# Performance work log

Hardware: AMD Instinct MI355X
Metric: run time of the kernel (lower is better)

Reference implementation:

```python
import jax, jax.numpy as jnp
import numpy as np

WINDOW = (2, 8, 8)  # (T, H, W); N = 128
NUM_HEADS = 6
DIM = 192


def _relative_position_index(ws):
    """NxN int index into the relative-position-bias table (faithful port)."""
    d, h, w = np.meshgrid(np.arange(ws[0]), np.arange(ws[1]), np.arange(ws[2]), indexing='ij')
    coords = np.stack([d, h, w]).reshape(3, -1)            # (3, N)
    rel = coords[:, :, None] - coords[:, None, :]          # (3, N, N)
    rel = rel.transpose(1, 2, 0).astype(np.int64)          # (N, N, 3)
    rel[:, :, 0] += ws[0] - 1
    rel[:, :, 1] += ws[1] - 1
    rel[:, :, 2] += ws[2] - 1
    rel[:, :, 0] *= (2 * ws[1] - 1) * (2 * ws[2] - 1)
    rel[:, :, 1] *= 2 * ws[2] - 1
    return rel.sum(-1)                                     # (N, N)


def setup_inputs() -> dict:
    key = jax.random.key(0)
    k1, k2, k3, k4, k5, k6 = jax.random.split(key, 6)
    N = WINDOW[0] * WINDOW[1] * WINDOW[2]                  # 128
    B_ = 1024                                              # num_windows * batch
    nW = 64
    table_len = (2 * WINDOW[0] - 1) * (2 * WINDOW[1] - 1) * (2 * WINDOW[2] - 1)  # 675
    x = jax.random.normal(k1, (B_, N, DIM), dtype=jnp.float32)
    mask = jax.random.normal(k2, (nW, N, N), dtype=jnp.float32)  # additive attn mask
    qkv_w = jax.random.normal(k3, (3 * DIM, DIM), dtype=jnp.float32) * 0.02
    proj_w = jax.random.normal(k4, (DIM, DIM), dtype=jnp.float32) * 0.02
    proj_b = jax.random.normal(k5, (DIM,), dtype=jnp.float32) * 0.02
    rpb_table = jax.random.normal(k6, (table_len, NUM_HEADS), dtype=jnp.float32) * 0.02
    rel_index = jnp.asarray(_relative_position_index(WINDOW), dtype=jnp.int32)
    return {"x": x, "mask": mask, "qkv_w": qkv_w, "proj_w": proj_w,
            "proj_b": proj_b, "rpb_table": rpb_table, "rel_index": rel_index}


def reference(x, mask, qkv_w, proj_w, proj_b, rpb_table, rel_index):
    B_, N, C = x.shape
    H = NUM_HEADS
    hd = C // H
    scale = hd ** (-0.5)
    # qkv projection (no bias, qkv_bias=False)
    qkv = (x @ qkv_w.T).reshape(B_, N, 3, H, hd)
    q, k, v = qkv[:, :, 0], qkv[:, :, 1], qkv[:, :, 2]      # (B_, N, H, hd)
    # windowed attention scores
    attn = jnp.einsum('bnhd,bmhd->bhnm', q * scale, k)      # (B_, H, N, N)
    # gathered relative-position bias: (N, N, H) -> (H, N, N)
    bias = rpb_table[rel_index.reshape(-1)].reshape(N, N, H).transpose(2, 0, 1)
    attn = attn + bias[None]
    # shift-window mask: (nW, N, N) broadcast over batch groups and heads
    nW = mask.shape[0]
    attn = attn.reshape(B_ // nW, nW, H, N, N) + mask[None, :, None]
    attn = attn.reshape(B_, H, N, N)
    attn = jax.nn.softmax(attn, axis=-1)
    out = jnp.einsum('bhnm,bmhd->bnhd', attn, v).reshape(B_, N, C)
    return out @ proj_w.T + proj_b
```

## Files before the change

kernel.cpp:

```cpp
#include <hip/hip_runtime.h>
#include <hip/hip_bf16.h>


typedef float f32x4 __attribute__((ext_vector_type(4)));
typedef short short8 __attribute__((ext_vector_type(8)));
typedef short short4e __attribute__((ext_vector_type(4)));

#define SCALE 0.17677669529663687f
#define LOG2E 1.4426950408889634f
#define QSC (SCALE * LOG2E)

static __device__ __forceinline__ short f2bf(float f) {
  __hip_bfloat16 h = __float2bfloat16(f);
  return __builtin_bit_cast(short, h);
}
static __device__ __forceinline__ f32x4 mfma16(short8 a, short8 b, f32x4 c) {
  return __builtin_amdgcn_mfma_f32_16x16x32_bf16(a, b, c, 0, 0, 0);
}

__global__ __launch_bounds__(256) void prep_w(const float* __restrict__ qkvw,
                                              const float* __restrict__ projw,
                                              short* __restrict__ wbf,
                                              short* __restrict__ pwbf) {
  int t = blockIdx.x * 256 + threadIdx.x;
  const int NQ = 27648;
  float4 f; short* dst;
  if (t < NQ) { f = ((const float4*)qkvw)[t]; dst = wbf + t * 4; }
  else        { f = ((const float4*)projw)[t - NQ]; dst = pwbf + (t - NQ) * 4; }
  short4e o; o[0] = f2bf(f.x); o[1] = f2bf(f.y); o[2] = f2bf(f.z); o[3] = f2bf(f.w);
  *(short4e*)dst = o;
}

__global__ __launch_bounds__(256) void prep_bm(const int* __restrict__ rel,
                                               const float* __restrict__ table,
                                               const float* __restrict__ mask,
                                               float* __restrict__ bmF) {
  int blk = blockIdx.x;
  int h = blk >> 6, w = blk & 63;
  int tid = threadIdx.x, lane = tid & 63, wave = tid >> 6;
  int lr = lane & 15, r4 = (lane >> 4) * 4;
  const float* mk = mask + (size_t)w * 16384;
  float* dst = bmF + (size_t)blk * 16384;
#pragma unroll
  for (int L = 0; L < 16; ++L) {
    int rf = L >> 3, rg = (L >> 1) & 3, cp = L & 1;
    int row = wave * 32 + rf * 16 + r4 + rg;
    float4 v;
#pragma unroll
    for (int e = 0; e < 4; ++e) {
      int col = (cp * 4 + e) * 16 + lr;
      float bias = table[rel[row * 128 + col] * 6 + h];
      ((float*)&v)[e] = (bias + mk[row * 128 + col]) * LOG2E;
    }
    ((float4*)dst)[L * 256 + tid] = v;
  }
}

__global__ __launch_bounds__(256, 2) void qkv_kernel(const float* __restrict__ x,
                                                     const short* __restrict__ wbf,
                                                     short* __restrict__ qb,
                                                     short* __restrict__ kb,
                                                     short* __restrict__ vb) {
  __shared__ short xt[24576];
  __shared__ short wt[2][6144];
  const int b = blockIdx.x, tid = threadIdx.x;
  const int wave = tid >> 6, lane = tid & 63;
  const int lr = lane & 15, g = lane >> 4;
  const int g16 = g * 16, r4 = g * 4;
  const int rowbase = wave * 32;
  const int xorkey = (lr & 7) << 4;
  char* xtb = (char*)xt;
  char* wtb = (char*)wt;

  int wsoff[3], wdoff[3];
#pragma unroll
  for (int i = 0; i < 3; ++i) {
    int idx8 = i * 256 + tid;
    int r = idx8 / 24, c = idx8 - r * 24;
    wsoff[i] = idx8 * 8;
    wdoff[i] = r * 384 + ((c * 16) ^ ((r & 7) << 4));
  }
  short8 wreg[3];
#pragma unroll
  for (int i = 0; i < 3; ++i) wreg[i] = *(const short8*)(wbf + wsoff[i]);

  const float4* xr = (const float4*)(x + (size_t)b * 24576);
  for (int s = tid; s < 6144; s += 256) {
    float4 f = xr[s];
    int r = s / 48, c8 = s - r * 48;
    int off = r * 384 + ((c8 * 8) ^ ((r & 7) << 4));
    short4e o; o[0] = f2bf(f.x); o[1] = f2bf(f.y); o[2] = f2bf(f.z); o[3] = f2bf(f.w);
    *(short4e*)(xtb + off) = o;
  }
#pragma unroll
  for (int i = 0; i < 3; ++i) *(short8*)(wtb + wdoff[i]) = wreg[i];
  __syncthreads();

  const int rA0 = (rowbase + lr) * 384, rA1 = rA0 + 16 * 384;
  const int wB0 = lr * 384, wB1 = wB0 + 16 * 384;

  for (int ch = 0; ch < 18; ++ch) {
    if (ch < 17) {
#pragma unroll
      for (int i = 0; i < 3; ++i)
        wreg[i] = *(const short8*)(wbf + (ch + 1) * 6144 + wsoff[i]);
    }
    const char* wbuf = wtb + (ch & 1) * 12288;
    f32x4 acc[2][2];
    acc[0][0] = acc[0][1] = acc[1][0] = acc[1][1] = f32x4{0.f, 0.f, 0.f, 0.f};
    const bool isv = (ch >= 12);
#pragma unroll
    for (int ks = 0; ks < 6; ++ks) {
      int cx = (ks * 64 + g16) ^ xorkey;
      short8 xa0 = *(const short8*)(xtb + rA0 + cx);
      short8 xa1 = *(const short8*)(xtb + rA1 + cx);
      short8 wf0 = *(const short8*)(wbuf + wB0 + cx);
      short8 wf1 = *(const short8*)(wbuf + wB1 + cx);
      if (!isv) {
        acc[0][0] = mfma16(xa0, wf0, acc[0][0]);
        acc[0][1] = mfma16(xa0, wf1, acc[0][1]);
        acc[1][0] = mfma16(xa1, wf0, acc[1][0]);
        acc[1][1] = mfma16(xa1, wf1, acc[1][1]);
      } else {
        acc[0][0] = mfma16(wf0, xa0, acc[0][0]);
        acc[0][1] = mfma16(wf0, xa1, acc[0][1]);
        acc[1][0] = mfma16(wf1, xa0, acc[1][0]);
        acc[1][1] = mfma16(wf1, xa1, acc[1][1]);
      }
    }
    if (!isv) {
      int h = (ch < 6) ? ch : ch - 6;
      short* dst = (ch < 6) ? qb : kb;
      float sc = (ch < 6) ? QSC : 1.0f;
      size_t base = ((size_t)b * 6 + h) * 4096;
#pragma unroll
      for (int rf = 0; rf < 2; ++rf)
#pragma unroll
        for (int cf = 0; cf < 2; ++cf) {
          int d = cf * 16 + lr;
#pragma unroll
          for (int rg = 0; rg < 4; ++rg) {
            int tok = rowbase + rf * 16 + r4 + rg;
            dst[base + (size_t)tok * 32 + d] = f2bf(acc[rf][cf][rg] * sc);
          }
        }
    } else {
      int h = ch - 12;
      size_t base = ((size_t)b * 6 + h) * 4096;
#pragma unroll
      for (int jf = 0; jf < 2; ++jf)
#pragma unroll
        for (int tf = 0; tf < 2; ++tf) {
          int tok = rowbase + tf * 16 + lr;
#pragma unroll
          for (int rg = 0; rg < 4; ++rg) {
            int d = jf * 16 + r4 + rg;
            vb[base + (size_t)d * 128 + tok] = f2bf(acc[jf][tf][rg]);
          }
        }
    }
    if (ch < 17) {
#pragma unroll
      for (int i = 0; i < 3; ++i)
        *(short8*)(wtb + ((ch + 1) & 1) * 12288 + wdoff[i]) = wreg[i];
      __syncthreads();
    }
  }
}

__global__ __launch_bounds__(256, 5) void attn_kernel(const short* __restrict__ qb,
                                                      const short* __restrict__ kb,
                                                      const short* __restrict__ vb,
                                                      const float* __restrict__ bmF,
                                                      char* __restrict__ outc) {
  __shared__ short p_lds[16384];
  char* pbuf = (char*)p_lds;
  const int bh = blockIdx.x, b = bh / 6, h = bh - b * 6;
  const short* qt = qb + (size_t)bh * 4096;
  const short* kt = kb + (size_t)bh * 4096;
  const short* vt = vb + (size_t)bh * 4096;
  const float4* bm4 = (const float4*)(bmF + ((size_t)h * 64 + (b & 63)) * 16384);
  short* outSlot = (short*)(outc + (size_t)b * 98304 + 49152);
  const int tid = threadIdx.x, wave = tid >> 6, lane = tid & 63;
  const int lr = lane & 15, g = lane >> 4, lkb = g * 8, r4 = g * 4;
  const int rowbase = wave * 32;

  float inv[2][4];
#pragma unroll
  for (int rf = 0; rf < 2; ++rf) {
    short8 a0 = *(const short8*)&qt[(rowbase + rf * 16 + lr) * 32 + lkb];
    f32x4 s[8];
    __builtin_amdgcn_s_setprio(1);
#pragma unroll
    for (int cf = 0; cf < 8; ++cf) {
      short8 bb = *(const short8*)&kt[(cf * 16 + lr) * 32 + lkb];
      f32x4 z = {0.f, 0.f, 0.f, 0.f};
      s[cf] = mfma16(a0, bb, z);
    }
    __builtin_amdgcn_s_setprio(0);
#pragma unroll
    for (int rg = 0; rg < 4; ++rg) {
      int L = rf * 8 + rg * 2;
      float4 bb0 = bm4[L * 256 + tid];
      float4 bb1 = bm4[(L + 1) * 256 + tid];
      float p0 = exp2f(s[0][rg] + bb0.x);
      float p1 = exp2f(s[1][rg] + bb0.y);
      float p2 = exp2f(s[2][rg] + bb0.z);
      float p3 = exp2f(s[3][rg] + bb0.w);
      float p4 = exp2f(s[4][rg] + bb1.x);
      float p5 = exp2f(s[5][rg] + bb1.y);
      float p6 = exp2f(s[6][rg] + bb1.z);
      float p7 = exp2f(s[7][rg] + bb1.w);
      float sum = ((p0 + p1) + (p2 + p3)) + ((p4 + p5) + (p6 + p7));
#pragma unroll
      for (int o = 1; o < 16; o <<= 1) sum += __shfl_xor(sum, o);
      inv[rf][rg] = 1.0f / sum;
      int row = rowbase + rf * 16 + r4 + rg;
      int base = (row << 8) + (lr << 1);
      int swz = (row & 15) << 4;
      *(short*)(pbuf + ((base + 0 * 32) ^ swz)) = f2bf(p0);
      *(short*)(pbuf + ((base + 1 * 32) ^ swz)) = f2bf(p1);
      *(short*)(pbuf + ((base + 2 * 32) ^ swz)) = f2bf(p2);
      *(short*)(pbuf + ((base + 3 * 32) ^ swz)) = f2bf(p3);
      *(short*)(pbuf + ((base + 4 * 32) ^ swz)) = f2bf(p4);
      *(short*)(pbuf + ((base + 5 * 32) ^ swz)) = f2bf(p5);
      *(short*)(pbuf + ((base + 6 * 32) ^ swz)) = f2bf(p6);
      *(short*)(pbuf + ((base + 7 * 32) ^ swz)) = f2bf(p7);
    }
  }
  const int rsw = lr << 4;
  f32x4 o[2][2];
  o[0][0] = o[0][1] = o[1][0] = o[1][1] = f32x4{0.f, 0.f, 0.f, 0.f};
#pragma unroll
  for (int ks = 0; ks < 4; ++ks) {
    int ra = ((rowbase + lr) << 8) + (ks << 6) + (g << 4);
    short8 pa0 = *(const short8*)(pbuf + ((ra) ^ rsw));
    short8 pa1 = *(const short8*)(pbuf + ((ra + (16 << 8)) ^ rsw));
    short8 b0 = *(const short8*)&vt[lr * 128 + ks * 32 + lkb];
    short8 b1 = *(const short8*)&vt[(16 + lr) * 128 + ks * 32 + lkb];
    __builtin_amdgcn_s_setprio(1);
    o[0][0] = mfma16(pa0, b0, o[0][0]);
    o[0][1] = mfma16(pa0, b1, o[0][1]);
    o[1][0] = mfma16(pa1, b0, o[1][0]);
    o[1][1] = mfma16(pa1, b1, o[1][1]);
    __builtin_amdgcn_s_setprio(0);
  }
#pragma unroll
  for (int rf = 0; rf < 2; ++rf)
#pragma unroll
    for (int cf = 0; cf < 2; ++cf)
#pragma unroll
      for (int rg = 0; rg < 4; ++rg) {
        int tok = rowbase + rf * 16 + r4 + rg;
        int d = cf * 16 + lr;
        outSlot[tok * 192 + h * 32 + d] = f2bf(o[rf][cf][rg] * inv[rf][rg]);
      }
}

__global__ __launch_bounds__(256, 2) void proj_kernel(const short* __restrict__ pwbf,
                                                      const float* __restrict__ pb,
                                                      float* __restrict__ out) {
  __shared__ short at[24576];
  __shared__ short wt[2][6144];
  const int b = blockIdx.x, tid = threadIdx.x;
  const int wave = tid >> 6, lane = tid & 63;
  const int lr = lane & 15, g = lane >> 4;
  const int g16 = g * 16, r4 = g * 4;
  const int rowbase = wave * 32;
  const int xorkey = (lr & 7) << 4;
  char* atb = (char*)at;
  char* wtb = (char*)wt;

  int wsoff[3], wdoff[3];
#pragma unroll
  for (int i = 0; i < 3; ++i) {
    int idx8 = i * 256 + tid;
    int r = idx8 / 24, c = idx8 - r * 24;
    wsoff[i] = idx8 * 8;
    wdoff[i] = r * 384 + ((c * 16) ^ ((r & 7) << 4));
  }
  short8 wreg[3];
#pragma unroll
  for (int i = 0; i < 3; ++i) wreg[i] = *(const short8*)(pwbf + wsoff[i]);

  const short8* ar = (const short8*)((const char*)out + (size_t)b * 98304 + 49152);
#pragma unroll
  for (int i = 0; i < 12; ++i) {
    int idx8 = i * 256 + tid;
    int r = idx8 / 24, c = idx8 - r * 24;
    short8 v = ar[idx8];
    *(short8*)(atb + r * 384 + ((c * 16) ^ ((r & 7) << 4))) = v;
  }
#pragma unroll
  for (int i = 0; i < 3; ++i) *(short8*)(wtb + wdoff[i]) = wreg[i];
  __syncthreads();

  const int rA0 = (rowbase + lr) * 384, rA1 = rA0 + 16 * 384;
  const int wB0 = lr * 384, wB1 = wB0 + 16 * 384;

  for (int ch = 0; ch < 6; ++ch) {
    if (ch < 5) {
#pragma unroll
      for (int i = 0; i < 3; ++i)
        wreg[i] = *(const short8*)(pwbf + (ch + 1) * 6144 + wsoff[i]);
    }
    const char* wbuf = wtb + (ch & 1) * 12288;
    f32x4 acc[2][2];
    acc[0][0] = acc[0][1] = acc[1][0] = acc[1][1] = f32x4{0.f, 0.f, 0.f, 0.f};
#pragma unroll
    for (int ks = 0; ks < 6; ++ks) {
      int cx = (ks * 64 + g16) ^ xorkey;
      short8 xa0 = *(const short8*)(atb + rA0 + cx);
      short8 xa1 = *(const short8*)(atb + rA1 + cx);
      short8 wf0 = *(const short8*)(wbuf + wB0 + cx);
      short8 wf1 = *(const short8*)(wbuf + wB1 + cx);
      acc[0][0] = mfma16(xa0, wf0, acc[0][0]);
      acc[0][1] = mfma16(xa0, wf1, acc[0][1]);
      acc[1][0] = mfma16(xa1, wf0, acc[1][0]);
      acc[1][1] = mfma16(xa1, wf1, acc[1][1]);
    }
#pragma unroll
    for (int cf = 0; cf < 2; ++cf) {
      int j = ch * 32 + cf * 16 + lr;
      float bj = pb[j];
#pragma unroll
      for (int rf = 0; rf < 2; ++rf)
#pragma unroll
        for (int rg = 0; rg < 4; ++rg) {
          int tok = rowbase + rf * 16 + r4 + rg;
          out[((size_t)b * 128 + tok) * 192 + j] = acc[rf][cf][rg] + bj;
        }
    }
    if (ch < 5) {
#pragma unroll
      for (int i = 0; i < 3; ++i)
        *(short8*)(wtb + ((ch + 1) & 1) * 12288 + wdoff[i]) = wreg[i];
      __syncthreads();
    }
  }
}

extern "C" void kernel_launch(void* const* d_in, const int* in_sizes, int n_in,
                              void* d_out, int out_size, void* d_ws, size_t ws_size,
                              hipStream_t stream) {
  const float* x      = (const float*)d_in[0];
  const float* mask   = (const float*)d_in[1];
  const float* qkv_w  = (const float*)d_in[2];
  const float* proj_w = (const float*)d_in[3];
  const float* proj_b = (const float*)d_in[4];
  const float* table  = (const float*)d_in[5];
  const int*   rel    = (const int*)d_in[6];
  char* ws = (char*)d_ws;
  size_t o = 0;
  float* bmF  = (float*)(ws + o); o += 25165824;
  short* wbf  = (short*)(ws + o); o += 221184;
  short* pwbf = (short*)(ws + o); o += 73728;
  short* qbp  = (short*)(ws + o); o += 50331648;
  short* kbp  = (short*)(ws + o); o += 50331648;
  short* vbp  = (short*)(ws + o); o += 50331648;
  float* out = (float*)d_out;

  prep_w<<<144, 256, 0, stream>>>(qkv_w, proj_w, wbf, pwbf);
  prep_bm<<<384, 256, 0, stream>>>(rel, table, mask, bmF);
  qkv_kernel<<<1024, 256, 0, stream>>>(x, wbf, qbp, kbp, vbp);
  attn_kernel<<<6144, 256, 0, stream>>>(qbp, kbp, vbp, bmF, (char*)d_out);
  proj_kernel<<<1024, 256, 0, stream>>>(pwbf, proj_b, out);
}
```

Before: 201.7 us.

## Keep x fragments in registers, transpose MFMA operands, loop heads per attention block

```diff
diff --git a/kernel.cpp b/kernel.cpp
--- a/kernel.cpp
+++ b/kernel.cpp
@@ -36,19 +36,19 @@
                                                const float* __restrict__ mask,
                                                float* __restrict__ bmF) {
   int blk = blockIdx.x;
-  int h = blk >> 6, w = blk & 63;
+  int w = blk / 6, h = blk - w * 6;
   int tid = threadIdx.x, lane = tid & 63, wave = tid >> 6;
-  int lr = lane & 15, r4 = (lane >> 4) * 4;
+  int lr = lane & 15, g = lane >> 4;
   const float* mk = mask + (size_t)w * 16384;
   float* dst = bmF + (size_t)blk * 16384;
 #pragma unroll
   for (int L = 0; L < 16; ++L) {
-    int rf = L >> 3, rg = (L >> 1) & 3, cp = L & 1;
-    int row = wave * 32 + rf * 16 + r4 + rg;
+    int qf = L >> 3, kf = L & 7;
+    int row = wave * 32 + qf * 16 + lr;
     float4 v;
 #pragma unroll
     for (int e = 0; e < 4; ++e) {
-      int col = (cp * 4 + e) * 16 + lr;
+      int col = kf * 16 + g * 4 + e;
       float bias = table[rel[row * 128 + col] * 6 + h];
       ((float*)&v)[e] = (bias + mk[row * 128 + col]) * LOG2E;
     }
@@ -56,21 +56,18 @@
   }
 }
 
-__global__ __launch_bounds__(256, 2) void qkv_kernel(const float* __restrict__ x,
+__global__ __launch_bounds__(256, 4) void qkv_kernel(const float* __restrict__ x,
                                                      const short* __restrict__ wbf,
                                                      short* __restrict__ qb,
                                                      short* __restrict__ kb,
                                                      short* __restrict__ vb) {
-  __shared__ short xt[24576];
   __shared__ short wt[2][6144];
+  char* wtb = (char*)wt;
   const int b = blockIdx.x, tid = threadIdx.x;
   const int wave = tid >> 6, lane = tid & 63;
-  const int lr = lane & 15, g = lane >> 4;
-  const int g16 = g * 16, r4 = g * 4;
+  const int lr = lane & 15, g = lane >> 4, g8 = g * 8, r4 = g * 4;
   const int rowbase = wave * 32;
   const int xorkey = (lr & 7) << 4;
-  char* xtb = (char*)xt;
-  char* wtb = (char*)wt;
 
   int wsoff[3], wdoff[3];
 #pragma unroll
@@ -84,79 +81,73 @@
 #pragma unroll
   for (int i = 0; i < 3; ++i) wreg[i] = *(const short8*)(wbf + wsoff[i]);
 
-  const float4* xr = (const float4*)(x + (size_t)b * 24576);
-  for (int s = tid; s < 6144; s += 256) {
-    float4 f = xr[s];
-    int r = s / 48, c8 = s - r * 48;
-    int off = r * 384 + ((c8 * 8) ^ ((r & 7) << 4));
-    short4e o; o[0] = f2bf(f.x); o[1] = f2bf(f.y); o[2] = f2bf(f.z); o[3] = f2bf(f.w);
-    *(short4e*)(xtb + off) = o;
+  short8 xa[2][6];
+  {
+    const float* xr = x + (size_t)b * 24576 + (size_t)(rowbase + lr) * 192;
+#pragma unroll
+    for (int tf = 0; tf < 2; ++tf)
+#pragma unroll
+      for (int ks = 0; ks < 6; ++ks) {
+        const float* p = xr + tf * 16 * 192 + ks * 32 + g8;
+        float4 f0 = *(const float4*)p;
+        float4 f1 = *(const float4*)(p + 4);
+        short8 v8;
+        v8[0] = f2bf(f0.x); v8[1] = f2bf(f0.y); v8[2] = f2bf(f0.z); v8[3] = f2bf(f0.w);
+        v8[4] = f2bf(f1.x); v8[5] = f2bf(f1.y); v8[6] = f2bf(f1.z); v8[7] = f2bf(f1.w);
+        xa[tf][ks] = v8;
+      }
   }
 #pragma unroll
   for (int i = 0; i < 3; ++i) *(short8*)(wtb + wdoff[i]) = wreg[i];
   __syncthreads();
 
-  const int rA0 = (rowbase + lr) * 384, rA1 = rA0 + 16 * 384;
-  const int wB0 = lr * 384, wB1 = wB0 + 16 * 384;
-
   for (int ch = 0; ch < 18; ++ch) {
     if (ch < 17) {
 #pragma unroll
       for (int i = 0; i < 3; ++i)
         wreg[i] = *(const short8*)(wbf + (ch + 1) * 6144 + wsoff[i]);
     }
-    const char* wbuf = wtb + (ch & 1) * 12288;
+    const char* wb = wtb + (ch & 1) * 12288;
     f32x4 acc[2][2];
     acc[0][0] = acc[0][1] = acc[1][0] = acc[1][1] = f32x4{0.f, 0.f, 0.f, 0.f};
-    const bool isv = (ch >= 12);
 #pragma unroll
     for (int ks = 0; ks < 6; ++ks) {
-      int cx = (ks * 64 + g16) ^ xorkey;
-      short8 xa0 = *(const short8*)(xtb + rA0 + cx);
-      short8 xa1 = *(const short8*)(xtb + rA1 + cx);
-      short8 wf0 = *(const short8*)(wbuf + wB0 + cx);
-      short8 wf1 = *(const short8*)(wbuf + wB1 + cx);
-      if (!isv) {
-        acc[0][0] = mfma16(xa0, wf0, acc[0][0]);
-        acc[0][1] = mfma16(xa0, wf1, acc[0][1]);
-        acc[1][0] = mfma16(xa1, wf0, acc[1][0]);
-        acc[1][1] = mfma16(xa1, wf1, acc[1][1]);
-      } else {
-        acc[0][0] = mfma16(wf0, xa0, acc[0][0]);
-        acc[0][1] = mfma16(wf0, xa1, acc[0][1]);
-        acc[1][0] = mfma16(wf1, xa0, acc[1][0]);
-        acc[1][1] = mfma16(wf1, xa1, acc[1][1]);
-      }
-    }
-    if (!isv) {
+      int cx = (ks * 64 + g * 16) ^ xorkey;
+      short8 w0 = *(const short8*)(wb + lr * 384 + cx);
+      short8 w1 = *(const short8*)(wb + (16 + lr) * 384 + cx);
+      acc[0][0] = mfma16(w0, xa[0][ks], acc[0][0]);
+      acc[0][1] = mfma16(w0, xa[1][ks], acc[0][1]);
+      acc[1][0] = mfma16(w1, xa[0][ks], acc[1][0]);
+      acc[1][1] = mfma16(w1, xa[1][ks], acc[1][1]);
+    }
+    if (ch < 12) {
+      short* dst = (ch < 6) ? qb : kb;
       int h = (ch < 6) ? ch : ch - 6;
-      short* dst = (ch < 6) ? qb : kb;
       float sc = (ch < 6) ? QSC : 1.0f;
       size_t base = ((size_t)b * 6 + h) * 4096;
 #pragma unroll
-      for (int rf = 0; rf < 2; ++rf)
-#pragma unroll
-        for (int cf = 0; cf < 2; ++cf) {
-          int d = cf * 16 + lr;
-#pragma unroll
-          for (int rg = 0; rg < 4; ++rg) {
-            int tok = rowbase + rf * 16 + r4 + rg;
-            dst[base + (size_t)tok * 32 + d] = f2bf(acc[rf][cf][rg] * sc);
-          }
+      for (int cf = 0; cf < 2; ++cf)
+#pragma unroll
+        for (int tf = 0; tf < 2; ++tf) {
+          int tok = rowbase + tf * 16 + lr;
+          short4e s4;
+          s4[0] = f2bf(acc[cf][tf][0] * sc);
+          s4[1] = f2bf(acc[cf][tf][1] * sc);
+          s4[2] = f2bf(acc[cf][tf][2] * sc);
+          s4[3] = f2bf(acc[cf][tf][3] * sc);
+          *(short4e*)&dst[base + (size_t)tok * 32 + cf * 16 + r4] = s4;
         }
     } else {
       int h = ch - 12;
       size_t base = ((size_t)b * 6 + h) * 4096;
 #pragma unroll
-      for (int jf = 0; jf < 2; ++jf)
+      for (int cf = 0; cf < 2; ++cf)
 #pragma unroll
         for (int tf = 0; tf < 2; ++tf) {
           int tok = rowbase + tf * 16 + lr;
 #pragma unroll
-          for (int rg = 0; rg < 4; ++rg) {
-            int d = jf * 16 + r4 + rg;
-            vb[base + (size_t)d * 128 + tok] = f2bf(acc[jf][tf][rg]);
-          }
+          for (int rg = 0; rg < 4; ++rg)
+            vb[base + (size_t)(cf * 16 + r4 + rg) * 128 + tok] = f2bf(acc[cf][tf][rg]);
         }
     }
     if (ch < 17) {
@@ -175,86 +166,80 @@
                                                       char* __restrict__ outc) {
   __shared__ short p_lds[16384];
   char* pbuf = (char*)p_lds;
-  const int bh = blockIdx.x, b = bh / 6, h = bh - b * 6;
-  const short* qt = qb + (size_t)bh * 4096;
-  const short* kt = kb + (size_t)bh * 4096;
-  const short* vt = vb + (size_t)bh * 4096;
-  const float4* bm4 = (const float4*)(bmF + ((size_t)h * 64 + (b & 63)) * 16384);
+  const int b = blockIdx.x;
+  const int tid = threadIdx.x, wave = tid >> 6, lane = tid & 63;
+  const int lr = lane & 15, g = lane >> 4, g8 = g * 8, r4 = g * 4;
+  const int rowbase = wave * 32;
+  const int swz = lr << 4;
   short* outSlot = (short*)(outc + (size_t)b * 98304 + 49152);
-  const int tid = threadIdx.x, wave = tid >> 6, lane = tid & 63;
-  const int lr = lane & 15, g = lane >> 4, lkb = g * 8, r4 = g * 4;
-  const int rowbase = wave * 32;
-
-  float inv[2][4];
-#pragma unroll
-  for (int rf = 0; rf < 2; ++rf) {
-    short8 a0 = *(const short8*)&qt[(rowbase + rf * 16 + lr) * 32 + lkb];
-    f32x4 s[8];
-    __builtin_amdgcn_s_setprio(1);
-#pragma unroll
-    for (int cf = 0; cf < 8; ++cf) {
-      short8 bb = *(const short8*)&kt[(cf * 16 + lr) * 32 + lkb];
-      f32x4 z = {0.f, 0.f, 0.f, 0.f};
-      s[cf] = mfma16(a0, bb, z);
-    }
-    __builtin_amdgcn_s_setprio(0);
-#pragma unroll
-    for (int rg = 0; rg < 4; ++rg) {
-      int L = rf * 8 + rg * 2;
-      float4 bb0 = bm4[L * 256 + tid];
-      float4 bb1 = bm4[(L + 1) * 256 + tid];
-      float p0 = exp2f(s[0][rg] + bb0.x);
-      float p1 = exp2f(s[1][rg] + bb0.y);
-      float p2 = exp2f(s[2][rg] + bb0.z);
-      float p3 = exp2f(s[3][rg] + bb0.w);
-      float p4 = exp2f(s[4][rg] + bb1.x);
-      float p5 = exp2f(s[5][rg] + bb1.y);
-      float p6 = exp2f(s[6][rg] + bb1.z);
-      float p7 = exp2f(s[7][rg] + bb1.w);
-      float sum = ((p0 + p1) + (p2 + p3)) + ((p4 + p5) + (p6 + p7));
-#pragma unroll
-      for (int o = 1; o < 16; o <<= 1) sum += __shfl_xor(sum, o);
-      inv[rf][rg] = 1.0f / sum;
-      int row = rowbase + rf * 16 + r4 + rg;
-      int base = (row << 8) + (lr << 1);
-      int swz = (row & 15) << 4;
-      *(short*)(pbuf + ((base + 0 * 32) ^ swz)) = f2bf(p0);
-      *(short*)(pbuf + ((base + 1 * 32) ^ swz)) = f2bf(p1);
-      *(short*)(pbuf + ((base + 2 * 32) ^ swz)) = f2bf(p2);
-      *(short*)(pbuf + ((base + 3 * 32) ^ swz)) = f2bf(p3);
-      *(short*)(pbuf + ((base + 4 * 32) ^ swz)) = f2bf(p4);
-      *(short*)(pbuf + ((base + 5 * 32) ^ swz)) = f2bf(p5);
-      *(short*)(pbuf + ((base + 6 * 32) ^ swz)) = f2bf(p6);
-      *(short*)(pbuf + ((base + 7 * 32) ^ swz)) = f2bf(p7);
-    }
-  }
-  const int rsw = lr << 4;
-  f32x4 o[2][2];
-  o[0][0] = o[0][1] = o[1][0] = o[1][1] = f32x4{0.f, 0.f, 0.f, 0.f};
-#pragma unroll
-  for (int ks = 0; ks < 4; ++ks) {
-    int ra = ((rowbase + lr) << 8) + (ks << 6) + (g << 4);
-    short8 pa0 = *(const short8*)(pbuf + ((ra) ^ rsw));
-    short8 pa1 = *(const short8*)(pbuf + ((ra + (16 << 8)) ^ rsw));
-    short8 b0 = *(const short8*)&vt[lr * 128 + ks * 32 + lkb];
-    short8 b1 = *(const short8*)&vt[(16 + lr) * 128 + ks * 32 + lkb];
-    __builtin_amdgcn_s_setprio(1);
-    o[0][0] = mfma16(pa0, b0, o[0][0]);
-    o[0][1] = mfma16(pa0, b1, o[0][1]);
-    o[1][0] = mfma16(pa1, b0, o[1][0]);
-    o[1][1] = mfma16(pa1, b1, o[1][1]);
-    __builtin_amdgcn_s_setprio(0);
-  }
-#pragma unroll
-  for (int rf = 0; rf < 2; ++rf)
-#pragma unroll
-    for (int cf = 0; cf < 2; ++cf)
-#pragma unroll
-      for (int rg = 0; rg < 4; ++rg) {
-        int tok = rowbase + rf * 16 + r4 + rg;
-        int d = cf * 16 + lr;
-        outSlot[tok * 192 + h * 32 + d] = f2bf(o[rf][cf][rg] * inv[rf][rg]);
+
+#pragma unroll 1
+  for (int h = 0; h < 6; ++h) {
+    const size_t bh = (size_t)b * 6 + h;
+    const short* qt = qb + bh * 4096;
+    const short* kt = kb + bh * 4096;
+    const short* vt = vb + bh * 4096;
+    const float4* bm4 = (const float4*)(bmF + ((size_t)(b & 63) * 6 + h) * 16384);
+    float inv[2];
+#pragma unroll
+    for (int qf = 0; qf < 2; ++qf) {
+      short8 qa = *(const short8*)&qt[(rowbase + qf * 16 + lr) * 32 + g8];
+      f32x4 s[8];
+      __builtin_amdgcn_s_setprio(1);
+#pragma unroll
+      for (int kf = 0; kf < 8; ++kf) {
+        short8 ka = *(const short8*)&kt[(kf * 16 + lr) * 32 + g8];
+        f32x4 z = {0.f, 0.f, 0.f, 0.f};
+        s[kf] = mfma16(ka, qa, z);
       }
+      __builtin_amdgcn_s_setprio(0);
+      float sum = 0.f;
+      const int rowb = (rowbase + qf * 16 + lr) << 8;
+#pragma unroll
+      for (int kf = 0; kf < 8; ++kf) {
+        float4 bm = bm4[(qf * 8 + kf) * 256 + tid];
+        float p0 = exp2f(s[kf][0] + bm.x);
+        float p1 = exp2f(s[kf][1] + bm.y);
+        float p2 = exp2f(s[kf][2] + bm.z);
+        float p3 = exp2f(s[kf][3] + bm.w);
+        sum += (p0 + p1) + (p2 + p3);
+        unsigned u0 = ((unsigned)(unsigned short)f2bf(p1) << 16) | (unsigned short)f2bf(p0);
+        unsigned u1 = ((unsigned)(unsigned short)f2bf(p3) << 16) | (unsigned short)f2bf(p2);
+        int2 wv; wv.x = (int)u0; wv.y = (int)u1;
+        *(int2*)(pbuf + ((rowb + kf * 32 + g * 8) ^ swz)) = wv;
+      }
+      sum += __shfl_xor(sum, 16);
+      sum += __shfl_xor(sum, 32);
+      inv[qf] = 1.0f / sum;
+    }
+    f32x4 o_[2][2];
+    o_[0][0] = o_[0][1] = o_[1][0] = o_[1][1] = f32x4{0.f, 0.f, 0.f, 0.f};
+#pragma unroll
+    for (int ks = 0; ks < 4; ++ks) {
+      short8 va0 = *(const short8*)&vt[lr * 128 + ks * 32 + g8];
+      short8 va1 = *(const short8*)&vt[(16 + lr) * 128 + ks * 32 + g8];
+      short8 pb0 = *(const short8*)(pbuf + ((((rowbase + lr) << 8) + ks * 64 + g * 16) ^ swz));
+      short8 pb1 = *(const short8*)(pbuf + ((((rowbase + 16 + lr) << 8) + ks * 64 + g * 16) ^ swz));
+      __builtin_amdgcn_s_setprio(1);
+      o_[0][0] = mfma16(va0, pb0, o_[0][0]);
+      o_[0][1] = mfma16(va0, pb1, o_[0][1]);
+      o_[1][0] = mfma16(va1, pb0, o_[1][0]);
+      o_[1][1] = mfma16(va1, pb1, o_[1][1]);
+      __builtin_amdgcn_s_setprio(0);
+    }
+#pragma unroll
+    for (int df = 0; df < 2; ++df)
+#pragma unroll
+      for (int tf = 0; tf < 2; ++tf) {
+        int tok = rowbase + tf * 16 + lr;
+        short4e s4;
+        s4[0] = f2bf(o_[df][tf][0] * inv[tf]);
+        s4[1] = f2bf(o_[df][tf][1] * inv[tf]);
+        s4[2] = f2bf(o_[df][tf][2] * inv[tf]);
+        s4[3] = f2bf(o_[df][tf][3] * inv[tf]);
+        *(short4e*)(outSlot + (size_t)tok * 192 + h * 32 + df * 16 + r4) = s4;
+      }
+  }
 }
 
 __global__ __launch_bounds__(256, 2) void proj_kernel(const short* __restrict__ pwbf,
@@ -363,6 +348,6 @@
   prep_w<<<144, 256, 0, stream>>>(qkv_w, proj_w, wbf, pwbf);
   prep_bm<<<384, 256, 0, stream>>>(rel, table, mask, bmF);
   qkv_kernel<<<1024, 256, 0, stream>>>(x, wbf, qbp, kbp, vbp);
-  attn_kernel<<<6144, 256, 0, stream>>>(qbp, kbp, vbp, bmF, (char*)d_out);
-  proj_kernel<<<1024, 256, 0, stream>>>(pwbf, proj_b, out);
-}
+  attn_kernel<<<1024, 256, 0, stream>>>(qbp, kbp, vbp, bmF, (char*)d_out);
+  proj_kernel<<<1024, 256, 0, stream>>>(pwbf, proj_b, (float*)d_out);
+}
```

Measured after the change: 235.3 us. 16.6% more time.
